# Performance work log

Hardware: AMD Instinct MI355X
Metric: run time of the kernel (lower is better)

The kernel has to match this reference:

```python
import jax, jax.numpy as jnp
import numpy as np

EMBED_DIM = 1024
NUM_HEADS = 16
HEAD_DIM = EMBED_DIM // NUM_HEADS


def setup_inputs() -> dict:
    key = jax.random.key(0)
    kq, kk, kv, kw1, kw2 = jax.random.split(key, 5)
    B, S, D = 4, 2048, EMBED_DIM
    # xavier_uniform with gain=0.1
    lim_qkv = 0.1 * np.sqrt(6.0 / (D + 3 * D))
    lim_out = 0.1 * np.sqrt(6.0 / (D + D))
    return {
        "query": jax.random.normal(kq, (B, S, D), dtype=jnp.float32),
        "key": jax.random.normal(kk, (B, S, D), dtype=jnp.float32),
        "value": jax.random.normal(kv, (B, S, D), dtype=jnp.float32),
        "W_qkv": jax.random.uniform(kw1, (3 * D, D), jnp.float32, -lim_qkv, lim_qkv),
        "b_qkv": jnp.zeros((3 * D,), jnp.float32),
        "W_out": jax.random.uniform(kw2, (D, D), jnp.float32, -lim_out, lim_out),
        "b_out": jnp.zeros((D,), jnp.float32),
    }


def reference(query, key, value, W_qkv, b_qkv, W_out, b_out):
    # NOTE: the torch module computes Q,K,V all from `query` (self-attention);
    # `key`/`value` args are API placeholders and unused in the math.
    B, S, D = query.shape
    qkv = query @ W_qkv.T + b_qkv                     # [B,S,3D]
    qkv = qkv.reshape(B, S, 3, NUM_HEADS, HEAD_DIM)
    q = qkv[:, :, 0].transpose(0, 2, 1, 3)            # [B,H,S,hd]
    k = qkv[:, :, 1].transpose(0, 2, 1, 3)
    v = qkv[:, :, 2].transpose(0, 2, 1, 3)
    scale = 1.0 / np.sqrt(HEAD_DIM)
    scores = jnp.einsum("bhqd,bhkd->bhqk", q, k) * scale
    attn = jax.nn.softmax(scores, axis=-1)
    out = jnp.einsum("bhqk,bhkd->bhqd", attn, v)      # [B,H,S,hd]
    out = out.transpose(0, 2, 1, 3).reshape(B, S, D)
    return out @ W_out.T + b_out
```

## Files before the change

### kernel.cpp

```cpp
#include <hip/hip_runtime.h>

typedef __attribute__((ext_vector_type(8))) __bf16 bf16x8;
typedef __attribute__((ext_vector_type(4))) float f32x4;
typedef unsigned short u16;
typedef unsigned int u32;

__device__ __forceinline__ u16 f2bf(float x) {
  u32 u = __builtin_bit_cast(u32, x);
  u = (u + 0x7FFFu + ((u >> 16) & 1u)) >> 16;
  return (u16)u;
}

#define BAR()                          \
  {                                    \
    asm volatile("" ::: "memory");     \
    __builtin_amdgcn_s_barrier();      \
    asm volatile("" ::: "memory");     \
  }

__global__ __launch_bounds__(256) void cvt3(
    const float* __restrict__ q, const float* __restrict__ w1,
    const float* __restrict__ w2, u16* __restrict__ oq, u16* __restrict__ ow1,
    u16* __restrict__ ow2) {
  int i = blockIdx.x * 256 + threadIdx.x;
  const float* in;
  u16* out;
  int base;
  if (i < 1048576) {
    in = q; out = oq; base = i;
  } else if (i < 1441792) {
    in = w1; out = ow1; base = i - 1048576;
  } else {
    in = w2; out = ow2; base = i - 1441792;
  }
  const float4* p = reinterpret_cast<const float4*>(in) + (size_t)base * 2;
  float4 a = p[0], b = p[1];
  uint4 r;
  r.x = (u32)f2bf(a.x) | ((u32)f2bf(a.y) << 16);
  r.y = (u32)f2bf(a.z) | ((u32)f2bf(a.w) << 16);
  r.z = (u32)f2bf(b.x) | ((u32)f2bf(b.y) << 16);
  r.w = (u32)f2bf(b.z) | ((u32)f2bf(b.w) << 16);
  reinterpret_cast<uint4*>(out)[base] = r;
}

__global__ __launch_bounds__(512, 2) void gemm_qkv8(
    const u16* __restrict__ A, const u16* __restrict__ Bw,
    const float* __restrict__ bias, u16* __restrict__ Qh,
    u16* __restrict__ Kh, u16* __restrict__ Vt) {
  constexpr int K = 1024;
  constexpr int NT = 16;
  __shared__ u16 Als[2][2][128][64];
  __shared__ u16 Bls[2][2][128][64];
  u16* const ALp = &Als[0][0][0][0];
  u16* const BLp = &Bls[0][0][0][0];

  const int tid = threadIdx.x;
  const int w = tid >> 6, l = tid & 63;
  const int kg = l >> 4, lr = l & 15;
  const int wr = w >> 2, wc = w & 3;
  const int bid = blockIdx.x;
  const int wg = (bid & 7) * 48 + (bid >> 3);
  const int tm = wg / 12, tn = wg % 12;

  const int r0 = tid >> 3, c0 = tid & 7;
  const int lc0 = c0 ^ (r0 & 7);
  const int ldsOff0 = tid * 8, ldsOff1 = tid * 8 + 4096;
  const u16* aSrc0[2];
  const u16* bSrc0[2];
#pragma unroll
  for (int h = 0; h < 2; ++h) {
    aSrc0[h] = A + (size_t)(tm * 256 + h * 128 + r0) * K + lc0 * 8;
    bSrc0[h] = Bw + (size_t)(tn * 256 + h * 128 + r0) * K + lc0 * 8;
  }
  const size_t rowStep = (size_t)64 * K;

#define ISSUE_A(BUF, H, T)                                                      \
  {                                                                             \
    __builtin_amdgcn_global_load_lds(                                           \
        (const __attribute__((address_space(1))) void*)(aSrc0[H] + (T) * 64),   \
        (__attribute__((address_space(3))) void*)(ALp + (BUF) * 16384 +         \
                                                 (H) * 8192 + ldsOff0),         \
        16, 0, 0);                                                              \
    __builtin_amdgcn_global_load_lds(                                           \
        (const __attribute__((address_space(1))) void*)(aSrc0[H] + rowStep +    \
                                                        (T) * 64),              \
        (__attribute__((address_space(3))) void*)(ALp + (BUF) * 16384 +         \
                                                 (H) * 8192 + ldsOff1),         \
        16, 0, 0);                                                              \
  }
#define ISSUE_B(BUF, H, T)                                                      \
  {                                                                             \
    __builtin_amdgcn_global_load_lds(                                           \
        (const __attribute__((address_space(1))) void*)(bSrc0[H] + (T) * 64),   \
        (__attribute__((address_space(3))) void*)(BLp + (BUF) * 16384 +         \
                                                 (H) * 8192 + ldsOff0),         \
        16, 0, 0);                                                              \
    __builtin_amdgcn_global_load_lds(                                           \
        (const __attribute__((address_space(1))) void*)(bSrc0[H] + rowStep +    \
                                                        (T) * 64),              \
        (__attribute__((address_space(3))) void*)(BLp + (BUF) * 16384 +         \
                                                 (H) * 8192 + ldsOff1),         \
        16, 0, 0);                                                              \
  }

  const int x7 = lr & 7;
  const int pc0 = (kg ^ x7) * 8;
  const int pc1 = ((kg + 4) ^ x7) * 8;
  const int wr16lr = wr * 16 + lr;
  const int wc16lr = wc * 16 + lr;

  const f32x4 fz = {0.f, 0.f, 0.f, 0.f};
  f32x4 acc[8][4];
#pragma unroll
  for (int m = 0; m < 8; ++m)
#pragma unroll
    for (int n = 0; n < 4; ++n) acc[m][n] = fz;

  bf16x8 aF[4][2], bF[2][2];

#define READ_A(P, MH)                                                           \
  {                                                                             \
    const u16* bp = ALp + (P) * 16384 + (MH) * 8192;                            \
    _Pragma("unroll") for (int mi = 0; mi < 4; ++mi) {                          \
      const u16* rp = bp + (mi * 32 + wr16lr) * 64;                             \
      aF[mi][0] = *(const bf16x8*)(rp + pc0);                                   \
      aF[mi][1] = *(const bf16x8*)(rp + pc1);                                   \
    }                                                                           \
  }
#define READ_B(P, NH)                                                           \
  {                                                                             \
    const u16* bp = BLp + (P) * 16384 + (NH) * 8192;                            \
    _Pragma("unroll") for (int ni = 0; ni < 2; ++ni) {                          \
      const u16* rp = bp + (ni * 64 + wc16lr) * 64;                             \
      bF[ni][0] = *(const bf16x8*)(rp + pc0);                                   \
      bF[ni][1] = *(const bf16x8*)(rp + pc1);                                   \
    }                                                                           \
  }
#define MFMA_Q(MH, NH)                                                          \
  {                                                                             \
    _Pragma("unroll") for (int mi = 0; mi < 4; ++mi)                            \
        _Pragma("unroll") for (int ni = 0; ni < 2; ++ni) {                      \
      acc[(MH)*4 + mi][(NH)*2 + ni] = __builtin_amdgcn_mfma_f32_16x16x32_bf16(  \
          aF[mi][0], bF[ni][0], acc[(MH)*4 + mi][(NH)*2 + ni], 0, 0, 0);        \
      acc[(MH)*4 + mi][(NH)*2 + ni] = __builtin_amdgcn_mfma_f32_16x16x32_bf16(  \
          aF[mi][1], bF[ni][1], acc[(MH)*4 + mi][(NH)*2 + ni], 0, 0, 0);        \
    }                                                                           \
  }

  ISSUE_A(0, 0, 0);
  ISSUE_A(0, 1, 0);
  ISSUE_B(0, 0, 0);
  ISSUE_B(0, 1, 0);
  ISSUE_A(1, 0, 1);
  ISSUE_B(1, 1, 1);

  for (int t = 0; t < NT; ++t) {
    const int p = t & 1;
    if (t == NT - 1) {
      asm volatile("s_waitcnt vmcnt(0)" ::: "memory");
    } else {
      asm volatile("s_waitcnt vmcnt(4)" ::: "memory");
    }
    BAR();
    if (t + 1 < NT) ISSUE_B(p ^ 1, 0, t + 1);
    READ_A(p, 0);
    READ_B(p, 0);
    BAR();
    __builtin_amdgcn_s_setprio(1);
    MFMA_Q(0, 0);
    __builtin_amdgcn_s_setprio(0);
    BAR();
    if (t + 1 < NT) ISSUE_A(p ^ 1, 1, t + 1);
    READ_B(p, 1);
    BAR();
    __builtin_amdgcn_s_setprio(1);
    MFMA_Q(0, 1);
    __builtin_amdgcn_s_setprio(0);
    BAR();
    if (t + 2 < NT) ISSUE_A(p, 0, t + 2);
    READ_A(p, 1);
    BAR();
    __builtin_amdgcn_s_setprio(1);
    MFMA_Q(1, 1);
    __builtin_amdgcn_s_setprio(0);
    BAR();
    if (t + 2 < NT) ISSUE_B(p, 1, t + 2);
    READ_B(p, 0);
    BAR();
    __builtin_amdgcn_s_setprio(1);
    MFMA_Q(1, 0);
    __builtin_amdgcn_s_setprio(0);
    BAR();
  }

#pragma unroll
  for (int m = 0; m < 8; ++m) {
    const int i0 = tm * 256 + m * 32 + wr * 16 + kg * 4;
    const int b = i0 >> 11, s0 = i0 & 2047;
#pragma unroll
    for (int n = 0; n < 4; ++n) {
      const int jc = tn * 256 + n * 64 + wc * 16 + lr;
      const float bs = bias[jc];
      const int sel = jc >> 10, hh = (jc >> 6) & 15, d = jc & 63;
      if (sel == 0) {
        u16* qp = Qh + ((size_t)((b * 16 + hh) * 2048 + s0)) * 64 + d;
#pragma unroll
        for (int j = 0; j < 4; ++j)
          qp[(size_t)j * 64] = f2bf((acc[m][n][j] + bs) * 0.18033688f);
      } else if (sel == 1) {
        u16* kp = Kh + ((size_t)((b * 16 + hh) * 2048 + s0)) * 64 + d;
#pragma unroll
        for (int j = 0; j < 4; ++j) kp[(size_t)j * 64] = f2bf(acc[m][n][j] + bs);
      } else {
        ushort4 vv;
        vv.x = f2bf(acc[m][n][0] + bs);
        vv.y = f2bf(acc[m][n][1] + bs);
        vv.z = f2bf(acc[m][n][2] + bs);
        vv.w = f2bf(acc[m][n][3] + bs);
        *(ushort4*)(Vt + ((size_t)((b * 16 + hh) * 64 + d)) * 2048 + s0) = vv;
      }
    }
  }
#undef ISSUE_A
#undef ISSUE_B
#undef READ_A
#undef READ_B
#undef MFMA_Q
}

__global__ __launch_bounds__(256) void gemm_out_k(
    const u16* __restrict__ A, const u16* __restrict__ Bw,
    const float* __restrict__ bias, float* __restrict__ Cout) {
  constexpr int N = 1024, K = 1024;
  __shared__ u16 As[128 * 32];
  __shared__ u16 Bs[128 * 32];
  const int tid = threadIdx.x;
  const int w = tid >> 6, l = tid & 63;
  const int kg = l >> 4, lr = l & 15;
  const int bid = blockIdx.x;
  const int wg = (bid & 7) * 64 + (bid >> 3);
  const int tm = wg >> 3, tn = wg & 7;
  const int wr = w >> 1, wc = w & 1;

  const u16* Ab = A + (size_t)tm * 128 * K;
  const u16* Bb = Bw + (size_t)tn * 128 * K;

  const f32x4 fz = {0.f, 0.f, 0.f, 0.f};
  f32x4 acc[4][4];
#pragma unroll
  for (int m = 0; m < 4; ++m)
#pragma unroll
    for (int n = 0; n < 4; ++n) acc[m][n] = fz;

  for (int k0 = 0; k0 < K; k0 += 32) {
#pragma unroll
    for (int u = 0; u < 2; ++u) {
      int e = u * 256 + tid;
      const u16* ga = Ab + (size_t)(e >> 2) * K + k0 + (e & 3) * 8;
      const u16* gb = Bb + (size_t)(e >> 2) * K + k0 + (e & 3) * 8;
      __builtin_amdgcn_global_load_lds(
          (const __attribute__((address_space(1))) void*)ga,
          (__attribute__((address_space(3))) void*)(As + (u * 256 + w * 64) * 8),
          16, 0, 0);
      __builtin_amdgcn_global_load_lds(
          (const __attribute__((address_space(1))) void*)gb,
          (__attribute__((address_space(3))) void*)(Bs + (u * 256 + w * 64) * 8),
          16, 0, 0);
    }
    asm volatile("s_waitcnt vmcnt(0)" ::: "memory");
    __syncthreads();
    bf16x8 a[4], b[4];
#pragma unroll
    for (int m = 0; m < 4; ++m)
      a[m] = *(const bf16x8*)(As + (wr * 64 + m * 16 + lr) * 32 + kg * 8);
#pragma unroll
    for (int n = 0; n < 4; ++n)
      b[n] = *(const bf16x8*)(Bs + (wc * 64 + n * 16 + lr) * 32 + kg * 8);
#pragma unroll
    for (int m = 0; m < 4; ++m)
#pragma unroll
      for (int n = 0; n < 4; ++n)
        acc[m][n] =
            __builtin_amdgcn_mfma_f32_16x16x32_bf16(a[m], b[n], acc[m][n], 0, 0, 0);
    __syncthreads();
  }

#pragma unroll
  for (int m = 0; m < 4; ++m) {
    const int i0 = tm * 128 + wr * 64 + m * 16 + kg * 4;
#pragma unroll
    for (int n = 0; n < 4; ++n) {
      const int jc = tn * 128 + wc * 64 + n * 16 + lr;
      const float bs = bias[jc];
#pragma unroll
      for (int j = 0; j < 4; ++j)
        Cout[(size_t)(i0 + j) * N + jc] = acc[m][n][j] + bs;
    }
  }
}

__global__ __launch_bounds__(256, 4) void attn_kernel(
    const u16* __restrict__ Qh, const u16* __restrict__ Kh,
    const u16* __restrict__ Vt, u16* __restrict__ Aout) {
  __shared__ alignas(16) u16 Kl[2][4096];
  __shared__ alignas(16) u16 Vl[2][4096];
  const int tid = threadIdx.x;
  const int w = tid >> 6, l = tid & 63;
  const int kg = l >> 4, lq = l & 15;
  const int bid = blockIdx.x;
  const int wgi = (bid & 7) * 128 + (bid >> 3);
  const int bh = wgi >> 4, qt = wgi & 15;
  const int qbase = qt * 128 + w * 32;

  const u16* Qb = Qh + ((size_t)(bh * 2048 + qbase + lq)) * 64;
  const bf16x8 aq00 = *(const bf16x8*)(Qb + kg * 8);
  const bf16x8 aq01 = *(const bf16x8*)(Qb + 32 + kg * 8);
  const bf16x8 aq10 = *(const bf16x8*)(Qb + 16 * 64 + kg * 8);
  const bf16x8 aq11 = *(const bf16x8*)(Qb + 16 * 64 + 32 + kg * 8);

  const u16* Kb = Kh + (size_t)bh * 2048 * 64;
  const u16* Vb = Vt + (size_t)bh * 64 * 2048;

  const int r7K = 4 * (lq >> 3) + (lq & 3);
  const int rowbK = 8 * ((lq >> 2) & 1) + r7K;
  const int ckK0 = (kg ^ r7K) * 8;
  const int ckK1 = ((kg + 4) ^ r7K) * 8;
  const int r7V = lq & 7;
  const int ckV0 = (kg ^ r7V) * 8;
  const int ckV1 = ((kg + 4) ^ r7V) * 8;

  bf16x8 vone;
#pragma unroll
  for (int i = 0; i < 8; ++i) vone[i] = (__bf16)1.0f;

  const f32x4 fz = {0.f, 0.f, 0.f, 0.f};
  f32x4 on0[4] = {fz, fz, fz, fz};
  f32x4 on1[4] = {fz, fz, fz, fz};
  f32x4 ls0 = fz, ls1 = fz;
  float m0 = -1e30f, m1 = -1e30f;

#define STAGE_KV(buf, kc)                                                        \
  {                                                                              \
    {                                                                            \
      const int s_ = tid, row_ = s_ >> 3, c_ = s_ & 7;                           \
      const int sw_ = (c_ ^ (row_ & 7)) * 8;                                     \
      const int srow_ = (row_ & ~20) | ((row_ & 4) << 2) | ((row_ & 16) >> 2);   \
      __builtin_amdgcn_global_load_lds(                                          \
          (const __attribute__((address_space(1))) void*)(Kb + (size_t)((kc) + srow_) * 64 + sw_), \
          (__attribute__((address_space(3))) void*)(&Kl[buf][s_ * 8]), 16, 0, 0);\
      __builtin_amdgcn_global_load_lds(                                          \
          (const __attribute__((address_space(1))) void*)(Vb + (size_t)row_ * 2048 + (kc) + sw_),  \
          (__attribute__((address_space(3))) void*)(&Vl[buf][s_ * 8]), 16, 0, 0);\
    }                                                                            \
    {                                                                            \
      const int s_ = 256 + tid, row_ = s_ >> 3, c_ = s_ & 7;                     \
      const int sw_ = (c_ ^ (row_ & 7)) * 8;                                     \
      const int srow_ = (row_ & ~20) | ((row_ & 4) << 2) | ((row_ & 16) >> 2);   \
      __builtin_amdgcn_global_load_lds(                                          \
          (const __attribute__((address_space(1))) void*)(Kb + (size_t)((kc) + srow_) * 64 + sw_), \
          (__attribute__((address_space(3))) void*)(&Kl[buf][s_ * 8]), 16, 0, 0);\
      __builtin_amdgcn_global_load_lds(                                          \
          (const __attribute__((address_space(1))) void*)(Vb + (size_t)row_ * 2048 + (kc) + sw_),  \
          (__attribute__((address_space(3))) void*)(&Vl[buf][s_ * 8]), 16, 0, 0);\
    }                                                                            \
  }

  STAGE_KV(0, 0);
  asm volatile("s_waitcnt vmcnt(0)" ::: "memory");
  __syncthreads();

  int cur = 0;
  for (int kc = 0; kc < 2048; kc += 64) {
    if (kc + 64 < 2048) STAGE_KV(cur ^ 1, kc + 64);
    const u16* Klc = Kl[cur];
    const u16* Vlc = Vl[cur];

    f32x4 st0[4], st1[4];
    __builtin_amdgcn_s_setprio(1);
#pragma unroll
    for (int t = 0; t < 4; ++t) {
      const int ro = (rowbK + ((t >> 1) * 32 + (t & 1) * 16)) * 64;
      bf16x8 k0 = *(const bf16x8*)(Klc + ro + ckK0);
      bf16x8 k1 = *(const bf16x8*)(Klc + ro + ckK1);
      f32x4 z0 = fz, z1 = fz;
      z0 = __builtin_amdgcn_mfma_f32_16x16x32_bf16(k0, aq00, z0, 0, 0, 0);
      z0 = __builtin_amdgcn_mfma_f32_16x16x32_bf16(k1, aq01, z0, 0, 0, 0);
      z1 = __builtin_amdgcn_mfma_f32_16x16x32_bf16(k0, aq10, z1, 0, 0, 0);
      z1 = __builtin_amdgcn_mfma_f32_16x16x32_bf16(k1, aq11, z1, 0, 0, 0);
      st0[t] = z0;
      st1[t] = z1;
    }
    __builtin_amdgcn_s_setprio(0);

    float rm0, rm1;
    rm0 = fmaxf(fmaxf(st0[0][0], st0[0][1]), st0[0][2]);
    rm0 = fmaxf(fmaxf(rm0, st0[0][3]), st0[1][0]);
    rm0 = fmaxf(fmaxf(rm0, st0[1][1]), st0[1][2]);
    rm0 = fmaxf(fmaxf(rm0, st0[1][3]), st0[2][0]);
    rm0 = fmaxf(fmaxf(rm0, st0[2][1]), st0[2][2]);
    rm0 = fmaxf(fmaxf(rm0, st0[2][3]), st0[3][0]);
    rm0 = fmaxf(fmaxf(rm0, st0[3][1]), st0[3][2]);
    rm0 = fmaxf(rm0, st0[3][3]);
    rm1 = fmaxf(fmaxf(st1[0][0], st1[0][1]), st1[0][2]);
    rm1 = fmaxf(fmaxf(rm1, st1[0][3]), st1[1][0]);
    rm1 = fmaxf(fmaxf(rm1, st1[1][1]), st1[1][2]);
    rm1 = fmaxf(fmaxf(rm1, st1[1][3]), st1[2][0]);
    rm1 = fmaxf(fmaxf(rm1, st1[2][1]), st1[2][2]);
    rm1 = fmaxf(fmaxf(rm1, st1[2][3]), st1[3][0]);
    rm1 = fmaxf(fmaxf(rm1, st1[3][1]), st1[3][2]);
    rm1 = fmaxf(rm1, st1[3][3]);
    rm0 = fmaxf(rm0, __shfl_xor(rm0, 16));
    rm0 = fmaxf(rm0, __shfl_xor(rm0, 32));
    rm1 = fmaxf(rm1, __shfl_xor(rm1, 16));
    rm1 = fmaxf(rm1, __shfl_xor(rm1, 32));
    if (!__all(fmaxf(rm0 - m0, rm1 - m1) <= 8.f)) {
      float mn0 = fmaxf(m0, rm0), mn1 = fmaxf(m1, rm1);
      float a0 = __builtin_amdgcn_exp2f(m0 - mn0);
      float a1 = __builtin_amdgcn_exp2f(m1 - mn1);
      m0 = mn0;
      m1 = mn1;
#pragma unroll
      for (int j = 0; j < 4; ++j) {
        float aj0 = __shfl(a0, kg * 4 + j);
        float aj1 = __shfl(a1, kg * 4 + j);
        ls0[j] *= aj0;
        ls1[j] *= aj1;
#pragma unroll
        for (int n = 0; n < 4; ++n) {
          on0[n][j] *= aj0;
          on1[n][j] *= aj1;
        }
      }
    }

    bf16x8 pa00, pa01, pa10, pa11;
#pragma unroll
    for (int j = 0; j < 4; ++j) {
      pa00[j] = (__bf16)__builtin_amdgcn_exp2f(st0[0][j] - m0);
      pa00[4 + j] = (__bf16)__builtin_amdgcn_exp2f(st0[1][j] - m0);
      pa01[j] = (__bf16)__builtin_amdgcn_exp2f(st0[2][j] - m0);
      pa01[4 + j] = (__bf16)__builtin_amdgcn_exp2f(st0[3][j] - m0);
      pa10[j] = (__bf16)__builtin_amdgcn_exp2f(st1[0][j] - m1);
      pa10[4 + j] = (__bf16)__builtin_amdgcn_exp2f(st1[1][j] - m1);
      pa11[j] = (__bf16)__builtin_amdgcn_exp2f(st1[2][j] - m1);
      pa11[4 + j] = (__bf16)__builtin_amdgcn_exp2f(st1[3][j] - m1);
    }

    __builtin_amdgcn_s_setprio(1);
    ls0 = __builtin_amdgcn_mfma_f32_16x16x32_bf16(pa00, vone, ls0, 0, 0, 0);
    ls0 = __builtin_amdgcn_mfma_f32_16x16x32_bf16(pa01, vone, ls0, 0, 0, 0);
    ls1 = __builtin_amdgcn_mfma_f32_16x16x32_bf16(pa10, vone, ls1, 0, 0, 0);
    ls1 = __builtin_amdgcn_mfma_f32_16x16x32_bf16(pa11, vone, ls1, 0, 0, 0);
#pragma unroll
    for (int n = 0; n < 4; ++n) {
      const int ro = (n * 16 + lq) * 64;
      bf16x8 v0 = *(const bf16x8*)(Vlc + ro + ckV0);
      bf16x8 v1 = *(const bf16x8*)(Vlc + ro + ckV1);
      on0[n] = __builtin_amdgcn_mfma_f32_16x16x32_bf16(pa00, v0, on0[n], 0, 0, 0);
      on0[n] = __builtin_amdgcn_mfma_f32_16x16x32_bf16(pa01, v1, on0[n], 0, 0, 0);
      on1[n] = __builtin_amdgcn_mfma_f32_16x16x32_bf16(pa10, v0, on1[n], 0, 0, 0);
      on1[n] = __builtin_amdgcn_mfma_f32_16x16x32_bf16(pa11, v1, on1[n], 0, 0, 0);
    }
    __builtin_amdgcn_s_setprio(0);

    asm volatile("s_waitcnt vmcnt(0)" ::: "memory");
    __syncthreads();
    cur ^= 1;
  }

  const int b = bh >> 4, h = bh & 15;
  {
    u16* Ob = Aout + (size_t)(b * 2048 + qbase + kg * 4) * 1024 + h * 64 + lq;
#pragma unroll
    for (int j = 0; j < 4; ++j) {
      float inv = 1.f / ls0[j];
#pragma unroll
      for (int n = 0; n < 4; ++n)
        Ob[(size_t)j * 1024 + n * 16] = f2bf(on0[n][j] * inv);
    }
  }
  {
    u16* Ob = Aout + (size_t)(b * 2048 + qbase + 16 + kg * 4) * 1024 + h * 64 + lq;
#pragma unroll
    for (int j = 0; j < 4; ++j) {
      float inv = 1.f / ls1[j];
#pragma unroll
      for (int n = 0; n < 4; ++n)
        Ob[(size_t)j * 1024 + n * 16] = f2bf(on1[n][j] * inv);
    }
  }
}

extern "C" void kernel_launch(void* const* d_in, const int* in_sizes, int n_in,
                              void* d_out, int out_size, void* d_ws, size_t ws_size,
                              hipStream_t stream) {
  const float* query = (const float*)d_in[0];
  const float* Wqkv = (const float*)d_in[3];
  const float* bqkv = (const float*)d_in[4];
  const float* Wout = (const float*)d_in[5];
  const float* bout = (const float*)d_in[6];
  float* out = (float*)d_out;

  char* ws = (char*)d_ws;
  u16* qx = (u16*)(ws);
  u16* wqkvb = (u16*)(ws + 16777216);
  u16* woutb = (u16*)(ws + 23068672);
  u16* Qh = (u16*)(ws + 25165824);
  u16* Kh = (u16*)(ws + 41943040);
  u16* Vt = (u16*)(ws + 58720256);
  u16* attn = qx;

  cvt3<<<6144, 256, 0, stream>>>(query, Wqkv, Wout, qx, wqkvb, woutb);

  gemm_qkv8<<<384, 512, 0, stream>>>(qx, wqkvb, bqkv, Qh, Kh, Vt);
  attn_kernel<<<1024, 256, 0, stream>>>(Qh, Kh, Vt, attn);
  gemm_out_k<<<512, 256, 0, stream>>>(attn, woutb, bout, out);
}
```

Baseline: 201.4 us.

## Replace pipelined 256x256 QKV GEMM with simple single-buffered 128x128 tile kernel

The QKV projection GEMM drops its 512-thread, double-buffered 256x256 tile kernel with interleaved barriers, setprio and prefetch. It now uses a 256-thread kernel with 128x128 tiles and a single LDS buffer, which waits for all loads and syncs on every K step. This gives more blocks (1536) and lower LDS and register use per block, possibly better occupancy. In exchange it loses the overlap of global loads with MFMA work and roughly doubles global traffic per output.

```diff
diff --git a/kernel.cpp b/kernel.cpp
--- a/kernel.cpp
+++ b/kernel.cpp
@@ -10,13 +10,6 @@
   u = (u + 0x7FFFu + ((u >> 16) & 1u)) >> 16;
   return (u16)u;
 }
-
-#define BAR()                          \
-  {                                    \
-    asm volatile("" ::: "memory");     \
-    __builtin_amdgcn_s_barrier();      \
-    asm volatile("" ::: "memory");     \
-  }
 
 __global__ __launch_bounds__(256) void cvt3(
     const float* __restrict__ q, const float* __restrict__ w1,
@@ -43,163 +36,85 @@
   reinterpret_cast<uint4*>(out)[base] = r;
 }
 
-__global__ __launch_bounds__(512, 2) void gemm_qkv8(
+__global__ __launch_bounds__(256) void gemm_qkv_bt(
     const u16* __restrict__ A, const u16* __restrict__ Bw,
     const float* __restrict__ bias, u16* __restrict__ Qh,
     u16* __restrict__ Kh, u16* __restrict__ Vt) {
   constexpr int K = 1024;
-  constexpr int NT = 16;
-  __shared__ u16 Als[2][2][128][64];
-  __shared__ u16 Bls[2][2][128][64];
-  u16* const ALp = &Als[0][0][0][0];
-  u16* const BLp = &Bls[0][0][0][0];
-
+  __shared__ u16 As[128 * 64];
+  __shared__ u16 Bs[128 * 64];
   const int tid = threadIdx.x;
   const int w = tid >> 6, l = tid & 63;
   const int kg = l >> 4, lr = l & 15;
-  const int wr = w >> 2, wc = w & 3;
   const int bid = blockIdx.x;
-  const int wg = (bid & 7) * 48 + (bid >> 3);
-  const int tm = wg / 12, tn = wg % 12;
-
-  const int r0 = tid >> 3, c0 = tid & 7;
-  const int lc0 = c0 ^ (r0 & 7);
-  const int ldsOff0 = tid * 8, ldsOff1 = tid * 8 + 4096;
-  const u16* aSrc0[2];
-  const u16* bSrc0[2];
-#pragma unroll
-  for (int h = 0; h < 2; ++h) {
-    aSrc0[h] = A + (size_t)(tm * 256 + h * 128 + r0) * K + lc0 * 8;
-    bSrc0[h] = Bw + (size_t)(tn * 256 + h * 128 + r0) * K + lc0 * 8;
-  }
-  const size_t rowStep = (size_t)64 * K;
-
-#define ISSUE_A(BUF, H, T)                                                      \
-  {                                                                             \
-    __builtin_amdgcn_global_load_lds(                                           \
-        (const __attribute__((address_space(1))) void*)(aSrc0[H] + (T) * 64),   \
-        (__attribute__((address_space(3))) void*)(ALp + (BUF) * 16384 +         \
-                                                 (H) * 8192 + ldsOff0),         \
-        16, 0, 0);                                                              \
-    __builtin_amdgcn_global_load_lds(                                           \
-        (const __attribute__((address_space(1))) void*)(aSrc0[H] + rowStep +    \
-                                                        (T) * 64),              \
-        (__attribute__((address_space(3))) void*)(ALp + (BUF) * 16384 +         \
-                                                 (H) * 8192 + ldsOff1),         \
-        16, 0, 0);                                                              \
-  }
-#define ISSUE_B(BUF, H, T)                                                      \
-  {                                                                             \
-    __builtin_amdgcn_global_load_lds(                                           \
-        (const __attribute__((address_space(1))) void*)(bSrc0[H] + (T) * 64),   \
-        (__attribute__((address_space(3))) void*)(BLp + (BUF) * 16384 +         \
-                                                 (H) * 8192 + ldsOff0),         \
-        16, 0, 0);                                                              \
-    __builtin_amdgcn_global_load_lds(                                           \
-        (const __attribute__((address_space(1))) void*)(bSrc0[H] + rowStep +    \
-                                                        (T) * 64),              \
-        (__attribute__((address_space(3))) void*)(BLp + (BUF) * 16384 +         \
-                                                 (H) * 8192 + ldsOff1),         \
-        16, 0, 0);                                                              \
-  }
+  const int wg = (bid & 7) * 192 + (bid >> 3);
+  const int tm = wg / 24, tn = wg % 24;
+  const int wr = w >> 1, wc = w & 1;
+
+  const u16* Ab = A + (size_t)tm * 128 * K;
+  const u16* Bb = Bw + (size_t)tn * 128 * K;
+
+  const int sr0 = tid >> 3, sc0 = tid & 7;
+
+#define GLL(SRC, DST)                                                   \
+  __builtin_amdgcn_global_load_lds(                                     \
+      (const __attribute__((address_space(1))) void*)(SRC),             \
+      (__attribute__((address_space(3))) void*)(DST), 16, 0, 0)
+
+  const f32x4 fz = {0.f, 0.f, 0.f, 0.f};
+  f32x4 acc[4][4];
+#pragma unroll
+  for (int m = 0; m < 4; ++m)
+#pragma unroll
+    for (int n = 0; n < 4; ++n) acc[m][n] = fz;
 
   const int x7 = lr & 7;
   const int pc0 = (kg ^ x7) * 8;
   const int pc1 = ((kg + 4) ^ x7) * 8;
-  const int wr16lr = wr * 16 + lr;
-  const int wc16lr = wc * 16 + lr;
-
-  const f32x4 fz = {0.f, 0.f, 0.f, 0.f};
-  f32x4 acc[8][4];
-#pragma unroll
-  for (int m = 0; m < 8; ++m)
-#pragma unroll
-    for (int n = 0; n < 4; ++n) acc[m][n] = fz;
-
-  bf16x8 aF[4][2], bF[2][2];
-
-#define READ_A(P, MH)                                                           \
-  {                                                                             \
-    const u16* bp = ALp + (P) * 16384 + (MH) * 8192;                            \
-    _Pragma("unroll") for (int mi = 0; mi < 4; ++mi) {                          \
-      const u16* rp = bp + (mi * 32 + wr16lr) * 64;                             \
-      aF[mi][0] = *(const bf16x8*)(rp + pc0);                                   \
-      aF[mi][1] = *(const bf16x8*)(rp + pc1);                                   \
-    }                                                                           \
-  }
-#define READ_B(P, NH)                                                           \
-  {                                                                             \
-    const u16* bp = BLp + (P) * 16384 + (NH) * 8192;                            \
-    _Pragma("unroll") for (int ni = 0; ni < 2; ++ni) {                          \
-      const u16* rp = bp + (ni * 64 + wc16lr) * 64;                             \
-      bF[ni][0] = *(const bf16x8*)(rp + pc0);                                   \
-      bF[ni][1] = *(const bf16x8*)(rp + pc1);                                   \
-    }                                                                           \
-  }
-#define MFMA_Q(MH, NH)                                                          \
-  {                                                                             \
-    _Pragma("unroll") for (int mi = 0; mi < 4; ++mi)                            \
-        _Pragma("unroll") for (int ni = 0; ni < 2; ++ni) {                      \
-      acc[(MH)*4 + mi][(NH)*2 + ni] = __builtin_amdgcn_mfma_f32_16x16x32_bf16(  \
-          aF[mi][0], bF[ni][0], acc[(MH)*4 + mi][(NH)*2 + ni], 0, 0, 0);        \
-      acc[(MH)*4 + mi][(NH)*2 + ni] = __builtin_amdgcn_mfma_f32_16x16x32_bf16(  \
-          aF[mi][1], bF[ni][1], acc[(MH)*4 + mi][(NH)*2 + ni], 0, 0, 0);        \
-    }                                                                           \
-  }
-
-  ISSUE_A(0, 0, 0);
-  ISSUE_A(0, 1, 0);
-  ISSUE_B(0, 0, 0);
-  ISSUE_B(0, 1, 0);
-  ISSUE_A(1, 0, 1);
-  ISSUE_B(1, 1, 1);
-
-  for (int t = 0; t < NT; ++t) {
-    const int p = t & 1;
-    if (t == NT - 1) {
-      asm volatile("s_waitcnt vmcnt(0)" ::: "memory");
-    } else {
-      asm volatile("s_waitcnt vmcnt(4)" ::: "memory");
-    }
-    BAR();
-    if (t + 1 < NT) ISSUE_B(p ^ 1, 0, t + 1);
-    READ_A(p, 0);
-    READ_B(p, 0);
-    BAR();
-    __builtin_amdgcn_s_setprio(1);
-    MFMA_Q(0, 0);
-    __builtin_amdgcn_s_setprio(0);
-    BAR();
-    if (t + 1 < NT) ISSUE_A(p ^ 1, 1, t + 1);
-    READ_B(p, 1);
-    BAR();
-    __builtin_amdgcn_s_setprio(1);
-    MFMA_Q(0, 1);
-    __builtin_amdgcn_s_setprio(0);
-    BAR();
-    if (t + 2 < NT) ISSUE_A(p, 0, t + 2);
-    READ_A(p, 1);
-    BAR();
-    __builtin_amdgcn_s_setprio(1);
-    MFMA_Q(1, 1);
-    __builtin_amdgcn_s_setprio(0);
-    BAR();
-    if (t + 2 < NT) ISSUE_B(p, 1, t + 2);
-    READ_B(p, 0);
-    BAR();
-    __builtin_amdgcn_s_setprio(1);
-    MFMA_Q(1, 0);
-    __builtin_amdgcn_s_setprio(0);
-    BAR();
-  }
-
-#pragma unroll
-  for (int m = 0; m < 8; ++m) {
-    const int i0 = tm * 256 + m * 32 + wr * 16 + kg * 4;
+
+  for (int k0 = 0; k0 < K; k0 += 64) {
+#pragma unroll
+    for (int u = 0; u < 4; ++u) {
+      const int s = u * 256 + tid;
+      const int row = u * 32 + sr0;
+      const int lc = sc0 ^ (row & 7);
+      GLL(Ab + (size_t)row * K + k0 + lc * 8, As + s * 8);
+      GLL(Bb + (size_t)row * K + k0 + lc * 8, Bs + s * 8);
+    }
+    asm volatile("s_waitcnt vmcnt(0)" ::: "memory");
+    __syncthreads();
+    bf16x8 a0[4], a1[4], b0[4], b1[4];
+#pragma unroll
+    for (int m = 0; m < 4; ++m) {
+      const u16* rp = As + (wr * 64 + m * 16 + lr) * 64;
+      a0[m] = *(const bf16x8*)(rp + pc0);
+      a1[m] = *(const bf16x8*)(rp + pc1);
+    }
+#pragma unroll
+    for (int n = 0; n < 4; ++n) {
+      const u16* rp = Bs + (wc * 64 + n * 16 + lr) * 64;
+      b0[n] = *(const bf16x8*)(rp + pc0);
+      b1[n] = *(const bf16x8*)(rp + pc1);
+    }
+#pragma unroll
+    for (int m = 0; m < 4; ++m)
+#pragma unroll
+      for (int n = 0; n < 4; ++n) {
+        acc[m][n] =
+            __builtin_amdgcn_mfma_f32_16x16x32_bf16(a0[m], b0[n], acc[m][n], 0, 0, 0);
+        acc[m][n] =
+            __builtin_amdgcn_mfma_f32_16x16x32_bf16(a1[m], b1[n], acc[m][n], 0, 0, 0);
+      }
+    __syncthreads();
+  }
+
+#pragma unroll
+  for (int m = 0; m < 4; ++m) {
+    const int i0 = tm * 128 + wr * 64 + m * 16 + kg * 4;
     const int b = i0 >> 11, s0 = i0 & 2047;
 #pragma unroll
     for (int n = 0; n < 4; ++n) {
-      const int jc = tn * 256 + n * 64 + wc * 16 + lr;
+      const int jc = tn * 128 + wc * 64 + n * 16 + lr;
       const float bs = bias[jc];
       const int sel = jc >> 10, hh = (jc >> 6) & 15, d = jc & 63;
       if (sel == 0) {
@@ -221,11 +136,7 @@
       }
     }
   }
-#undef ISSUE_A
-#undef ISSUE_B
-#undef READ_A
-#undef READ_B
-#undef MFMA_Q
+#undef GLL
 }
 
 __global__ __launch_bounds__(256) void gemm_out_k(
@@ -512,7 +423,7 @@
 
   cvt3<<<6144, 256, 0, stream>>>(query, Wqkv, Wout, qx, wqkvb, woutb);
 
-  gemm_qkv8<<<384, 512, 0, stream>>>(qx, wqkvb, bqkv, Qh, Kh, Vt);
+  gemm_qkv_bt<<<1536, 256, 0, stream>>>(qx, wqkvb, bqkv, Qh, Kh, Vt);
   attn_kernel<<<1024, 256, 0, stream>>>(Qh, Kh, Vt, attn);
   gemm_out_k<<<512, 256, 0, stream>>>(attn, woutb, bout, out);
 }
```

Result: faster. 187.9 us (-6.7%).
